# Optimization experiments

Measured on AMD Instinct MI355X. Metric: run time of the kernel, lower is better.

## Reference

```python
import jax, jax.numpy as jnp
import numpy as np

B, C, NP, NT, D = 512, 3, 49, 76, 768
EPS = 0.1        # Sinkhorn entropic regularization
THRESH = 0.01    # convergence threshold on mean |r - r0|
MAX_ITER = 100


def _normalize(x, axis=-1):
    n = jnp.linalg.norm(x, axis=axis, keepdims=True)
    return x / jnp.maximum(n, 1e-12)


def _sinkhorn(K, u, v):
    # K: [B, n, m], u: [B, n], v: [B, m]. Faithful to the torch loop with
    # early exit: do-while via lax.while_loop (err check after each update).
    def cond(state):
        _, _, err, i = state
        return (i < MAX_ITER) & (err >= THRESH)

    def body(state):
        r, c, _, i = state
        r_new = u / jnp.einsum('bnm,bm->bn', K, c)
        c_new = v / jnp.einsum('bnm,bn->bm', K, r_new)
        err = jnp.mean(jnp.abs(r_new - r))
        return (r_new, c_new, err, i + 1)

    r0 = jnp.ones_like(u)
    c0 = jnp.ones_like(v)
    r, c, _, _ = jax.lax.while_loop(
        cond, body, (r0, c0, jnp.asarray(jnp.inf, K.dtype), 0))
    return r[..., :, None] * c[..., None, :] * K  # transport plan T


def _cross_entropy(logits):
    # labels = arange(B) (diagonal targets)
    logp = jax.nn.log_softmax(logits, axis=-1)
    return -jnp.mean(jnp.diagonal(logp))


def setup_inputs() -> dict:
    key = jax.random.key(0)
    k1, k2, k3, k4 = jax.random.split(key, 4)
    return {
        'image_features': jax.random.normal(k1, (B, C, D), jnp.float32),
        'text_features': jax.random.normal(k2, (B, C, D), jnp.float32),
        'logit_scale': jnp.full((1,), 100.0, jnp.float32),
        'local_image_features': jax.random.normal(k3, (B, C, NP, D), jnp.float32),
        'local_text_features': jax.random.normal(k4, (B, C, NT, D), jnp.float32),
    }


def reference(image_features, text_features, logit_scale,
              local_image_features, local_text_features):
    scale = logit_scale.reshape(())
    li = _normalize(local_image_features)          # [B, C, 49, D]
    lt = _normalize(local_text_features)           # [B, C, 76, D]
    # per-channel token similarity: [B, C, 49, 76]
    sim = jnp.einsum('bcnd,bcmd->bcnm', li, lt)
    # Sinkhorn is under no_grad in the original -> stop_gradient on K and T.
    K = jax.lax.stop_gradient(jnp.exp(-(1.0 - sim) / EPS))
    u = jnp.full((B, NP), 1.0 / NP, sim.dtype)
    v = jnp.full((B, NT), 1.0 / NT, sim.dtype)
    ot_loss = jnp.asarray(0.0, sim.dtype)
    for ch in range(C):  # per-channel Sinkhorn (independent early stopping)
        T = jax.lax.stop_gradient(_sinkhorn(K[:, ch], u, v))
        ot_loss = ot_loss + jnp.sum(T * sim[:, ch])
    # logits averaged over the 3 channels (sum over c folded into einsum)
    logits_per_image = scale * jnp.einsum(
        'bcd,ncd->bn', image_features, text_features) / C
    logits_per_text = logits_per_image.T
    total_loss = (_cross_entropy(logits_per_image)
                  + _cross_entropy(logits_per_text)) / 2 + ot_loss
    return total_loss
```

## Files before the change

kernel.cpp:

```cpp
#include <hip/hip_runtime.h>

#define NB 512
#define NC 3
#define NP_ 49
#define NT_ 76
#define DD 768

typedef __attribute__((ext_vector_type(8))) short bf16x8;
typedef __attribute__((ext_vector_type(4))) float f32x4;

__device__ inline unsigned short f2bf(float x) {
    unsigned int u = __float_as_uint(x);
    u += 0x7FFFu + ((u >> 16) & 1u);
    return (unsigned short)(u >> 16);
}
__device__ inline float bfval(unsigned short s) {
    return __uint_as_float((unsigned int)s << 16);
}
__device__ inline float f4get(const float4& v, int e) {
    return e == 0 ? v.x : e == 1 ? v.y : e == 2 ? v.z : v.w;
}

__device__ inline bf16x8 pack8(const float4& lo, const float4& hi, float& nrm) {
    bf16x8 r;
    unsigned short s; float x;
    s = f2bf(lo.x); x = bfval(s); nrm += x * x; r[0] = (short)s;
    s = f2bf(lo.y); x = bfval(s); nrm += x * x; r[1] = (short)s;
    s = f2bf(lo.z); x = bfval(s); nrm += x * x; r[2] = (short)s;
    s = f2bf(lo.w); x = bfval(s); nrm += x * x; r[3] = (short)s;
    s = f2bf(hi.x); x = bfval(s); nrm += x * x; r[4] = (short)s;
    s = f2bf(hi.y); x = bfval(s); nrm += x * x; r[5] = (short)s;
    s = f2bf(hi.z); x = bfval(s); nrm += x * x; r[6] = (short)s;
    s = f2bf(hi.w); x = bfval(s); nrm += x * x; r[7] = (short)s;
    return r;
}

__global__ __launch_bounds__(64, 2) void sink_kernel(const float* __restrict__ lif,
                                                     const float* __restrict__ ltf,
                                                     float* __restrict__ out) {
    const int lane = threadIdx.x;
    const int bc   = blockIdx.x;
    const int lr = lane & 15, lk = lane >> 4;
    const float* ga = lif + (size_t)bc * (NP_ * DD);
    const float* gb = ltf + (size_t)bc * (NT_ * DD);

    __shared__ float Kmat[NP_ * 77];
    __shared__ __attribute__((aligned(16))) float c_vec[80];
    __shared__ __attribute__((aligned(16))) float r_vec[64];

    const float* pa[4];
#pragma unroll
    for (int tn = 0; tn < 4; ++tn) {
        int row = tn * 16 + lr; if (row > NP_ - 1) row = NP_ - 1;
        pa[tn] = ga + row * DD + lk * 8;
    }
    const float* pb[5];
#pragma unroll
    for (int j = 0; j < 5; ++j) {
        int row = j * 16 + lr; if (row > NT_ - 1) row = NT_ - 1;
        pb[j] = gb + row * DD + lk * 8;
    }

    f32x4 acc[4][5];
    const f32x4 zero4 = {0.f, 0.f, 0.f, 0.f};
#pragma unroll
    for (int tn = 0; tn < 4; ++tn)
#pragma unroll
        for (int j = 0; j < 5; ++j) acc[tn][j] = zero4;
    float na[4] = {0.f, 0.f, 0.f, 0.f};
    float nb[5] = {0.f, 0.f, 0.f, 0.f, 0.f};

#pragma unroll 1
    for (int cc = 0; cc < 24; ++cc) {
        const int off = cc * 32;
        float4 a0[4], a1[4], b0[5], b1[5];
#pragma unroll
        for (int tn = 0; tn < 4; ++tn) {
            a0[tn] = *(const float4*)(pa[tn] + off);
            a1[tn] = *(const float4*)(pa[tn] + off + 4);
        }
#pragma unroll
        for (int j = 0; j < 5; ++j) {
            b0[j] = *(const float4*)(pb[j] + off);
            b1[j] = *(const float4*)(pb[j] + off + 4);
        }
        bf16x8 af[4], bfr[5];
#pragma unroll
        for (int tn = 0; tn < 4; ++tn) af[tn] = pack8(a0[tn], a1[tn], na[tn]);
#pragma unroll
        for (int j = 0; j < 5; ++j)  bfr[j] = pack8(b0[j], b1[j], nb[j]);
#pragma unroll
        for (int tn = 0; tn < 4; ++tn)
#pragma unroll
            for (int j = 0; j < 5; ++j)
                acc[tn][j] = __builtin_amdgcn_mfma_f32_16x16x32_bf16(af[tn], bfr[j], acc[tn][j], 0, 0, 0);
    }

#pragma unroll
    for (int tn = 0; tn < 4; ++tn) {
        float v = na[tn];
        v += __shfl_xor(v, 16);
        v += __shfl_xor(v, 32);
        na[tn] = 1.0f / fmaxf(sqrtf(v), 1e-12f);
    }
#pragma unroll
    for (int j = 0; j < 5; ++j) {
        float v = nb[j];
        v += __shfl_xor(v, 16);
        v += __shfl_xor(v, 32);
        nb[j] = 1.0f / fmaxf(sqrtf(v), 1e-12f);
    }

#pragma unroll
    for (int tn = 0; tn < 4; ++tn)
#pragma unroll
        for (int rg = 0; rg < 4; ++rg) {
            const int n = tn * 16 + lk * 4 + rg;
            const float ia = __shfl(na[tn], lk * 4 + rg);
            if (n < NP_) {
#pragma unroll
                for (int j = 0; j < 5; ++j) {
                    const int m = j * 16 + lr;
                    if (m < NT_) {
                        const float simv = acc[tn][j][rg] * ia * nb[j];
                        Kmat[n * 77 + m] = __expf((simv - 1.0f) * 10.0f);
                    }
                }
            }
        }

    c_vec[lane] = 1.0f;
    if (lane < 16) c_vec[64 + lane] = 1.0f;

    const int nrow = (lane < NP_) ? lane : 0;
    float Kr[NT_];
#pragma unroll
    for (int m = 0; m < NT_; ++m)
        Kr[m] = (lane < NP_) ? Kmat[nrow * 77 + m] : 0.0f;

    const int col2 = (lane < 12) ? (64 + lane) : (NT_ - 1);
    float Kc[NP_], Kc2[NP_];
#pragma unroll
    for (int n = 0; n < NP_; ++n) {
        Kc[n]  = Kmat[n * 77 + lane];
        Kc2[n] = Kmat[n * 77 + col2];
    }

    float r_old = 1.0f;
    float err;
    int iter = 0;
    do {
        float y0 = 0.f, y1 = 0.f, y2 = 0.f, y3 = 0.f;
#pragma unroll
        for (int q = 0; q < 19; ++q) {
            const float4 cq = *(const float4*)(c_vec + q * 4);
#pragma unroll
            for (int e = 0; e < 4; ++e) {
                const int i = 4 * q + e;
                const float cv = f4get(cq, e);
                if (i < 19)      y0 += Kr[i] * cv;
                else if (i < 38) y1 += Kr[i] * cv;
                else if (i < 57) y2 += Kr[i] * cv;
                else             y3 += Kr[i] * cv;
            }
        }
        const float y  = (y0 + y1) + (y2 + y3);
        const float rn = (1.0f / 49.0f) / y;
        const float de = (lane < NP_) ? fabsf(rn - r_old) : 0.0f;
        r_old = rn;
        r_vec[lane] = rn;

        float e = de;
        e += __shfl_xor(e, 1);
        e += __shfl_xor(e, 2);
        e += __shfl_xor(e, 4);
        e += __shfl_xor(e, 8);
        const float g0 = __shfl(e, 0),  g1 = __shfl(e, 16);
        const float g2 = __shfl(e, 32), g3 = __shfl(e, 48);
        err = (((g0 + g1) + g2) + g3) * (1.0f / 49.0f);

        float z0 = 0.f, z1 = 0.f, w0 = 0.f, w1 = 0.f;
#pragma unroll
        for (int q = 0; q < 13; ++q) {
            const float4 rq = *(const float4*)(r_vec + q * 4);
#pragma unroll
            for (int e2 = 0; e2 < 4; ++e2) {
                const int n = 4 * q + e2;
                const float rv = f4get(rq, e2);
                if (n < 25)      { z0 += Kc[n] * rv; w0 += Kc2[n] * rv; }
                else if (n < 49) { z1 += Kc[n] * rv; w1 += Kc2[n] * rv; }
            }
        }
        c_vec[lane] = (1.0f / 76.0f) / (z0 + z1);
        if (lane < 12) c_vec[64 + lane] = (1.0f / 76.0f) / (w0 + w1);
        ++iter;
    } while (iter < 100 && err >= 1e-3f);

    float part = 0.f;
    if (lane < NP_) {
        const float rr = r_old;
#pragma unroll
        for (int q = 0; q < 19; ++q) {
            const float4 cq = *(const float4*)(c_vec + q * 4);
#pragma unroll
            for (int e2 = 0; e2 < 4; ++e2) {
                const float kv = Kr[4 * q + e2];
                part += rr * f4get(cq, e2) * kv * (__logf(kv) * 0.1f + 1.0f);
            }
        }
    }
#pragma unroll
    for (int o = 1; o < 64; o <<= 1) part += __shfl_xor(part, o);
    if (lane == 0) atomicAdd(out, part);
}

__global__ __launch_bounds__(256) void gemm_logits(const float* __restrict__ A,
                                                   const float* __restrict__ Bm,
                                                   float* __restrict__ L) {
    __shared__ __attribute__((aligned(16))) float At[64 * 36];
    __shared__ __attribute__((aligned(16))) float Bt[64 * 36];
    const int tid = threadIdx.x;
    const int i0 = blockIdx.x * 64, j0 = blockIdx.y * 64, kbase = blockIdx.z * 288;
    const int ty = tid >> 4, tx = tid & 15;
    float accv[4][4] = {};
    for (int kc = 0; kc < 9; ++kc) {
        int kb = kbase + kc * 32;
#pragma unroll
        for (int t = 0; t < 2; ++t) {
            int idx = tid + t * 256;
            int row = idx >> 3, q = idx & 7;
            *(float4*)(At + row * 36 + q * 4) =
                *(const float4*)(A + (size_t)(i0 + row) * 2304 + kb + q * 4);
            *(float4*)(Bt + row * 36 + q * 4) =
                *(const float4*)(Bm + (size_t)(j0 + row) * 2304 + kb + q * 4);
        }
        __syncthreads();
#pragma unroll 8
        for (int k = 0; k < 32; ++k) {
            float ra[4], rb[4];
#pragma unroll
            for (int a = 0; a < 4; ++a) ra[a] = At[(ty + 16 * a) * 36 + k];
#pragma unroll
            for (int b = 0; b < 4; ++b) rb[b] = Bt[(tx + 16 * b) * 36 + k];
#pragma unroll
            for (int a = 0; a < 4; ++a)
#pragma unroll
                for (int b = 0; b < 4; ++b) accv[a][b] += ra[a] * rb[b];
        }
        __syncthreads();
    }
#pragma unroll
    for (int a = 0; a < 4; ++a)
#pragma unroll
        for (int b = 0; b < 4; ++b)
            atomicAdd(L + (size_t)(i0 + ty + 16 * a) * 512 + (j0 + tx + 16 * b), accv[a][b]);
}

__device__ inline float blk_max(float v, float* sred, int wave, int lane) {
#pragma unroll
    for (int o = 1; o < 64; o <<= 1) v = fmaxf(v, __shfl_xor(v, o));
    if (lane == 0) sred[wave] = v;
    __syncthreads();
    v = fmaxf(fmaxf(sred[0], sred[1]), fmaxf(sred[2], sred[3]));
    __syncthreads();
    return v;
}
__device__ inline float blk_sum(float v, float* sred, int wave, int lane) {
#pragma unroll
    for (int o = 1; o < 64; o <<= 1) v += __shfl_xor(v, o);
    if (lane == 0) sred[wave] = v;
    __syncthreads();
    v = sred[0] + sred[1] + sred[2] + sred[3];
    __syncthreads();
    return v;
}

__global__ __launch_bounds__(256) void ce_kernel(const float* __restrict__ L,
                                                 const float* __restrict__ lsc,
                                                 float* __restrict__ out) {
    __shared__ float sred[4];
    const int i = blockIdx.x, tid = threadIdx.x;
    const int wave = tid >> 6, lane = tid & 63;
    const float s = lsc[0] * (1.0f / 3.0f);

    float xr0 = L[(size_t)i * 512 + tid] * s;
    float xr1 = L[(size_t)i * 512 + tid + 256] * s;
    float xc0 = L[(size_t)tid * 512 + i] * s;
    float xc1 = L[(size_t)(tid + 256) * 512 + i] * s;

    float mr = blk_max(fmaxf(xr0, xr1), sred, wave, lane);
    float sr = blk_sum(__expf(xr0 - mr) + __expf(xr1 - mr), sred, wave, lane);
    float lse_r = mr + __logf(sr);

    float mc = blk_max(fmaxf(xc0, xc1), sred, wave, lane);
    float sc = blk_sum(__expf(xc0 - mc) + __expf(xc1 - mc), sred, wave, lane);
    float lse_c = mc + __logf(sc);

    if (tid == 0) {
        float dii = L[(size_t)i * 512 + i] * s;
        atomicAdd(out, (lse_r + lse_c - 2.0f * dii) * (1.0f / 1024.0f));
    }
}

extern "C" void kernel_launch(void* const* d_in, const int* in_sizes, int n_in,
                              void* d_out, int out_size, void* d_ws, size_t ws_size,
                              hipStream_t stream) {
    const float* img = (const float*)d_in[0];
    const float* txt = (const float*)d_in[1];
    const float* lsc = (const float*)d_in[2];
    const float* lif = (const float*)d_in[3];
    const float* ltf = (const float*)d_in[4];
    float* out = (float*)d_out;
    float* Lws = (float*)d_ws;

    hipMemsetAsync(out, 0, sizeof(float), stream);
    hipMemsetAsync(Lws, 0, 512 * 512 * sizeof(float), stream);

    hipLaunchKernelGGL(gemm_logits, dim3(8, 8, 8), dim3(256), 0, stream, img, txt, Lws);
    hipLaunchKernelGGL(sink_kernel, dim3(NB * NC), dim3(64), 0, stream, lif, ltf, out);
    hipLaunchKernelGGL(ce_kernel, dim3(512), dim3(256), 0, stream, Lws, lsc, out);
}
```

Before: 669.5 us.

## Double-buffer global feature loads in registers to overlap with MFMA work

The similarity GEMM loop is restructured so that the next 32-column chunk of both feature matrices is loaded into a second register buffer while the current chunk is packed to bf16 and fed to MFMA. Per-row pointers are replaced with unsigned byte offsets from a single base pointer, which may let the compiler use cheaper offset addressing. The goal is to hide global-memory latency, which a single wave per block cannot otherwise cover. In exchange it roughly doubles the registers held for staged loads, which risks spills or lower occupancy.

```diff
diff --git a/kernel.cpp b/kernel.cpp
--- a/kernel.cpp
+++ b/kernel.cpp
@@ -35,30 +35,60 @@
     return r;
 }
 
+#define LOAD_CHUNK(Ra0, Ra1, Rb0, Rb1) do {                                   \
+    _Pragma("unroll")                                                         \
+    for (int f_ = 0; f_ < 4; ++f_) {                                          \
+        Ra0[f_] = *(const float4*)(gab + voA[f_]);                            \
+        Ra1[f_] = *(const float4*)(gab + voA[f_] + 16);                       \
+    }                                                                         \
+    _Pragma("unroll")                                                         \
+    for (int f_ = 0; f_ < 5; ++f_) {                                          \
+        Rb0[f_] = *(const float4*)(gbb + voB[f_]);                            \
+        Rb1[f_] = *(const float4*)(gbb + voB[f_] + 16);                       \
+    }                                                                         \
+    _Pragma("unroll")                                                         \
+    for (int f_ = 0; f_ < 4; ++f_) voA[f_] += 128;                            \
+    _Pragma("unroll")                                                         \
+    for (int f_ = 0; f_ < 5; ++f_) voB[f_] += 128;                            \
+} while (0)
+
+#define CONSUME(Ra0, Ra1, Rb0, Rb1) do {                                      \
+    bf16x8 bfr_[5];                                                           \
+    _Pragma("unroll")                                                         \
+    for (int j_ = 0; j_ < 5; ++j_) bfr_[j_] = pack8(Rb0[j_], Rb1[j_], nb[j_]);\
+    _Pragma("unroll")                                                         \
+    for (int tn_ = 0; tn_ < 4; ++tn_) {                                       \
+        bf16x8 af_ = pack8(Ra0[tn_], Ra1[tn_], na[tn_]);                      \
+        _Pragma("unroll")                                                     \
+        for (int j_ = 0; j_ < 5; ++j_)                                        \
+            acc[tn_][j_] = __builtin_amdgcn_mfma_f32_16x16x32_bf16(           \
+                af_, bfr_[j_], acc[tn_][j_], 0, 0, 0);                        \
+    }                                                                         \
+} while (0)
+
 __global__ __launch_bounds__(64, 2) void sink_kernel(const float* __restrict__ lif,
                                                      const float* __restrict__ ltf,
                                                      float* __restrict__ out) {
     const int lane = threadIdx.x;
     const int bc   = blockIdx.x;
     const int lr = lane & 15, lk = lane >> 4;
-    const float* ga = lif + (size_t)bc * (NP_ * DD);
-    const float* gb = ltf + (size_t)bc * (NT_ * DD);
+    const char* gab = (const char*)(lif + (size_t)bc * (NP_ * DD));
+    const char* gbb = (const char*)(ltf + (size_t)bc * (NT_ * DD));
 
     __shared__ float Kmat[NP_ * 77];
     __shared__ __attribute__((aligned(16))) float c_vec[80];
     __shared__ __attribute__((aligned(16))) float r_vec[64];
 
-    const float* pa[4];
+    unsigned voA[4], voB[5];
 #pragma unroll
     for (int tn = 0; tn < 4; ++tn) {
         int row = tn * 16 + lr; if (row > NP_ - 1) row = NP_ - 1;
-        pa[tn] = ga + row * DD + lk * 8;
-    }
-    const float* pb[5];
+        voA[tn] = (unsigned)(row * DD + lk * 8) * 4u;
+    }
 #pragma unroll
     for (int j = 0; j < 5; ++j) {
         int row = j * 16 + lr; if (row > NT_ - 1) row = NT_ - 1;
-        pb[j] = gb + row * DD + lk * 8;
+        voB[j] = (unsigned)(row * DD + lk * 8) * 4u;
     }
 
     f32x4 acc[4][5];
@@ -70,30 +100,16 @@
     float na[4] = {0.f, 0.f, 0.f, 0.f};
     float nb[5] = {0.f, 0.f, 0.f, 0.f, 0.f};
 
+    float4 xa0[4], xa1[4], xb0[5], xb1[5];
+    float4 ya0[4], ya1[4], yb0[5], yb1[5];
+
+    LOAD_CHUNK(xa0, xa1, xb0, xb1);
 #pragma unroll 1
-    for (int cc = 0; cc < 24; ++cc) {
-        const int off = cc * 32;
-        float4 a0[4], a1[4], b0[5], b1[5];
-#pragma unroll
-        for (int tn = 0; tn < 4; ++tn) {
-            a0[tn] = *(const float4*)(pa[tn] + off);
-            a1[tn] = *(const float4*)(pa[tn] + off + 4);
-        }
-#pragma unroll
-        for (int j = 0; j < 5; ++j) {
-            b0[j] = *(const float4*)(pb[j] + off);
-            b1[j] = *(const float4*)(pb[j] + off + 4);
-        }
-        bf16x8 af[4], bfr[5];
-#pragma unroll
-        for (int tn = 0; tn < 4; ++tn) af[tn] = pack8(a0[tn], a1[tn], na[tn]);
-#pragma unroll
-        for (int j = 0; j < 5; ++j)  bfr[j] = pack8(b0[j], b1[j], nb[j]);
-#pragma unroll
-        for (int tn = 0; tn < 4; ++tn)
-#pragma unroll
-            for (int j = 0; j < 5; ++j)
-                acc[tn][j] = __builtin_amdgcn_mfma_f32_16x16x32_bf16(af[tn], bfr[j], acc[tn][j], 0, 0, 0);
+    for (int cc = 0; cc < 24; cc += 2) {
+        LOAD_CHUNK(ya0, ya1, yb0, yb1);
+        CONSUME(xa0, xa1, xb0, xb1);
+        if (cc < 22) LOAD_CHUNK(xa0, xa1, xb0, xb1);
+        CONSUME(ya0, ya1, yb0, yb1);
     }
 
 #pragma unroll
```

After: 755.8 us. +12.9%, slower.
